# Optimization experiments

Measured on AMD Instinct MI355X. Metric: run time of the kernel, lower is better.

Reference implementation:

```python
import jax, jax.numpy as jnp
import numpy as np

B, S, C = 8, 2048, 1024
DROPOUT_RATE = 0.1


def setup_inputs() -> dict:
    key = jax.random.key(0)
    k1, k2, k3 = jax.random.split(key, 3)
    x = jax.random.normal(k1, (B, S, C), dtype=jnp.float32)
    # Fixed orthogonal projection buffer, as in __init__: U from SVD of a random matrix
    rand_mat = jax.random.normal(k2, (C, C), dtype=jnp.float32)
    U, _, _ = jnp.linalg.svd(rand_mat)
    U = U.astype(jnp.float32)
    # Base random permutation of [0, C)
    perm = jax.random.permutation(k3, C).astype(jnp.int32)
    # Stand-in for random.randint(0, 1000), fixed for determinism
    randint = 123
    return {"x": x, "U": U, "perm": perm, "randint": randint}


def reference(x, U, perm, randint):
    # channel_dim == -1, so the transpose in the original forward is a no-op.
    rand_scale = (DROPOUT_RATE / (1.0 - DROPOUT_RATE)) ** 0.5
    n = x.shape[-1]
    b = x.size // n
    # _randperm_like: per-row permutation ans[b_, i] = perm[i] * (6*randint*b_ + 1) mod n.
    # Reduce the multiplier mod n first so int32 arithmetic never overflows
    # (math is identical since (a*b) % n == (a*(b%n)) % n).
    batch_rand = (jnp.arange(b, dtype=jnp.int32) * (randint * 6) + 1) % n  # [b]
    ans = (perm[None, :] * batch_rand[:, None]) % n                        # [b, n]
    ans = ans.reshape(x.shape)                                             # same shape as x

    x_g = jnp.take_along_axis(x, ans, axis=-1)   # gather per-row permuted channels
    y = jnp.matmul(x_g, U)                        # shared (C,C) projection
    # scatter_(-1, ans, y) places y[..., j] at position ans[..., j]; since ans is a
    # permutation per row, this equals gathering y with the inverse permutation.
    inv = jnp.argsort(ans, axis=-1)
    x_next = jnp.take_along_axis(y, inv, axis=-1)
    return x_next * rand_scale + x
```

## Files before the change

kernel.cpp:

```cpp
#include <hip/hip_runtime.h>
#include <hip/hip_bf16.h>

#define WS_UT    ((size_t)0)
#define WS_XG    ((size_t)4*1024*1024)
#define WS_Y     ((size_t)36*1024*1024)

typedef __attribute__((ext_vector_type(8))) short short8;
typedef __attribute__((ext_vector_type(4))) float floatx4;

__device__ __forceinline__ void load_lds16(const void* g, void* l) {
  __builtin_amdgcn_global_load_lds(
      (const __attribute__((address_space(1))) void*)g,
      (__attribute__((address_space(3))) void*)l, 16, 0, 0);
}

__device__ __forceinline__ unsigned short f2bf(float f) {
  __hip_bfloat16 h = __float2bfloat16(f);
  return __builtin_bit_cast(unsigned short, h);
}
__device__ __forceinline__ float bf2f(unsigned short u) {
  return __uint_as_float(((unsigned)u) << 16);
}

__global__ void __launch_bounds__(256) prep_k(const float* __restrict__ U,
                                              unsigned short* __restrict__ ut) {
  __shared__ float tile[64][65];
  const int tn = (blockIdx.x & 15) * 64;
  const int tk = (blockIdx.x >> 4) * 64;
  const int r = threadIdx.x >> 6;
  const int c = threadIdx.x & 63;
  for (int s = 0; s < 16; ++s)
    tile[s * 4 + r][c] = U[(size_t)(tk + s * 4 + r) * 1024 + tn + c];
  __syncthreads();
  for (int s = 0; s < 16; ++s)
    ut[(size_t)(tn + s * 4 + r) * 1024 + tk + c] = f2bf(tile[c][s * 4 + r]);
}

__global__ void __launch_bounds__(256) gather_cast_k(const float* __restrict__ x,
                                                     const int* __restrict__ perm,
                                                     const int* __restrict__ prand,
                                                     unsigned short* __restrict__ xg) {
  __shared__ float xrow[4][1024];
  const int w = threadIdx.x >> 6, lane = threadIdx.x & 63;
  const int row = blockIdx.x * 4 + w;
  const unsigned mult = ((unsigned)prand[0] * 6u) & 1023u;
  const unsigned br = (((unsigned)row & 1023u) * mult + 1u) & 1023u;
  const float* xr = x + (size_t)row * 1024;
  unsigned short* xo = xg + (size_t)row * 1024;
  for (int t = 0; t < 4; ++t) {
    floatx4 v = *(const floatx4*)(xr + t * 256 + lane * 4);
    *(floatx4*)(&xrow[w][t * 256 + lane * 4]) = v;
  }
  __syncthreads();
  for (int t = 0; t < 4; ++t) {
    int i0 = t * 256 + lane * 4;
    int4 p = *(const int4*)(perm + i0);
    ushort4 o;
    o.x = f2bf(xrow[w][((unsigned)p.x * br) & 1023u]);
    o.y = f2bf(xrow[w][((unsigned)p.y * br) & 1023u]);
    o.z = f2bf(xrow[w][((unsigned)p.z * br) & 1023u]);
    o.w = f2bf(xrow[w][((unsigned)p.w * br) & 1023u]);
    *(ushort4*)(xo + i0) = o;
  }
}

__global__ void __launch_bounds__(256) gemm_k(const unsigned short* __restrict__ xg,
                                              const unsigned short* __restrict__ ut,
                                              unsigned short* __restrict__ y) {
  __shared__ __align__(16) char ldsA[16384];
  __shared__ __align__(16) char ldsB[16384];
  const int tid = threadIdx.x;
  const int w = tid >> 6, lane = tid & 63;
  const int l = blockIdx.x;
  const int xcd = l & 7;
  const int j = l >> 3;
  const int bn = (j & 7) * 128;
  const int bm = ((j >> 3) * 8 + xcd) * 128;
  const int wm = (w & 1) * 64, wn = (w >> 1) * 64;
  const int m = lane & 15, q = lane >> 4;
  const int srow = lane >> 3;
  const int sch = lane & 7;

  floatx4 acc[4][4];
  for (int i = 0; i < 4; ++i)
    for (int jj = 0; jj < 4; ++jj) acc[i][jj] = (floatx4)0.0f;

  for (int kt = 0; kt < 16; ++kt) {
    const int k0 = kt * 64;
    for (int t = 0; t < 4; ++t) {
      int row = w * 32 + t * 8 + srow;
      int sc = sch ^ (row & 7);
      load_lds16(xg + ((size_t)(bm + row) * 1024 + k0 + sc * 8),
                 ldsA + row * 128 + sch * 16);
      load_lds16(ut + ((size_t)(bn + row) * 1024 + k0 + sc * 8),
                 ldsB + row * 128 + sch * 16);
    }
    __syncthreads();
    for (int s = 0; s < 2; ++s) {
      short8 af[4], bfr[4];
      const int swz = ((s * 4 + q) ^ (m & 7)) * 16;
      for (int i = 0; i < 4; ++i)
        af[i] = *(const short8*)(ldsA + (wm + i * 16 + m) * 128 + swz);
      for (int jj = 0; jj < 4; ++jj)
        bfr[jj] = *(const short8*)(ldsB + (wn + jj * 16 + m) * 128 + swz);
      for (int i = 0; i < 4; ++i)
        for (int jj = 0; jj < 4; ++jj)
          acc[i][jj] = __builtin_amdgcn_mfma_f32_16x16x32_bf16(af[i], bfr[jj], acc[i][jj], 0, 0, 0);
    }
    __syncthreads();
  }
  for (int i = 0; i < 4; ++i) {
    int row = bm + wm + i * 16 + q * 4;
    for (int jj = 0; jj < 4; ++jj) {
      int col = bn + wn + jj * 16 + m;
      for (int r = 0; r < 4; ++r)
        y[(size_t)(row + r) * 1024 + col] = f2bf(acc[i][jj][r]);
    }
  }
}

__global__ void __launch_bounds__(256) scatter_out_k(const unsigned short* __restrict__ xg,
                                                     const unsigned short* __restrict__ y,
                                                     const int* __restrict__ perm,
                                                     const int* __restrict__ prand,
                                                     float* __restrict__ out) {
  __shared__ float obuf[4][1024];
  const int w = threadIdx.x >> 6, lane = threadIdx.x & 63;
  const int row = blockIdx.x * 4 + w;
  const unsigned mult = ((unsigned)prand[0] * 6u) & 1023u;
  const unsigned br = (((unsigned)row & 1023u) * mult + 1u) & 1023u;
  const unsigned short* yr = y + (size_t)row * 1024;
  const unsigned short* xr = xg + (size_t)row * 1024;
  for (int t = 0; t < 4; ++t) {
    int i0 = t * 256 + lane * 4;
    int4 p = *(const int4*)(perm + i0);
    ushort4 yv = *(const ushort4*)(yr + i0);
    ushort4 xv = *(const ushort4*)(xr + i0);
    obuf[w][((unsigned)p.x * br) & 1023u] = 0.3333333333333333f * bf2f(yv.x) + bf2f(xv.x);
    obuf[w][((unsigned)p.y * br) & 1023u] = 0.3333333333333333f * bf2f(yv.y) + bf2f(xv.y);
    obuf[w][((unsigned)p.z * br) & 1023u] = 0.3333333333333333f * bf2f(yv.z) + bf2f(xv.z);
    obuf[w][((unsigned)p.w * br) & 1023u] = 0.3333333333333333f * bf2f(yv.w) + bf2f(xv.w);
  }
  __syncthreads();
  float* orow = out + (size_t)row * 1024;
  for (int t = 0; t < 4; ++t) {
    int c0 = t * 256 + lane * 4;
    *(floatx4*)(orow + c0) = *(const floatx4*)(&obuf[w][c0]);
  }
}

extern "C" void kernel_launch(void* const* d_in, const int* in_sizes, int n_in,
                              void* d_out, int out_size, void* d_ws, size_t ws_size,
                              hipStream_t stream) {
  const float* x = (const float*)d_in[0];
  const float* U = (const float*)d_in[1];
  const int* perm = (const int*)d_in[2];
  const int* prand = (const int*)d_in[3];
  float* out = (float*)d_out;
  char* ws = (char*)d_ws;
  unsigned short* ut = (unsigned short*)(ws + WS_UT);
  unsigned short* xg = (unsigned short*)(ws + WS_XG);
  unsigned short* y = (unsigned short*)(ws + WS_Y);

  prep_k<<<256, 256, 0, stream>>>(U, ut);
  gather_cast_k<<<4096, 256, 0, stream>>>(x, perm, prand, xg);
  gemm_k<<<1024, 256, 0, stream>>>(xg, ut, y);
  scatter_out_k<<<4096, 256, 0, stream>>>(xg, y, perm, prand, out);
}
```

Before: 179.2 us.

## Fuse scatter-residual into GEMM epilogue and merge prep with gather kernel

The GEMM epilogue now writes fp32 outputs directly to their inverse-permuted positions, adding the residual from the original x, so the bf16 y intermediate and the separate scatter kernel are removed. The U transpose/cast and the row gather are combined into a single launch using block-index ranges. This cuts a full round trip of the intermediate through global memory and two launches. The cost is uncoalesced 4-byte scattered reads of x and writes of out in the epilogue.

New measurement: 235.8 us. 31.6% more time.

```diff
diff --git a/kernel.cpp b/kernel.cpp
--- a/kernel.cpp
+++ b/kernel.cpp
@@ -2,8 +2,7 @@
 #include <hip/hip_bf16.h>
 
 #define WS_UT    ((size_t)0)
-#define WS_XG    ((size_t)4*1024*1024)
-#define WS_Y     ((size_t)36*1024*1024)
+#define WS_XG    ((size_t)2*1024*1024)
 
 typedef __attribute__((ext_vector_type(8))) short short8;
 typedef __attribute__((ext_vector_type(4))) float floatx4;
@@ -18,31 +17,30 @@
   __hip_bfloat16 h = __float2bfloat16(f);
   return __builtin_bit_cast(unsigned short, h);
 }
-__device__ __forceinline__ float bf2f(unsigned short u) {
-  return __uint_as_float(((unsigned)u) << 16);
-}
 
-__global__ void __launch_bounds__(256) prep_k(const float* __restrict__ U,
-                                              unsigned short* __restrict__ ut) {
-  __shared__ float tile[64][65];
-  const int tn = (blockIdx.x & 15) * 64;
-  const int tk = (blockIdx.x >> 4) * 64;
-  const int r = threadIdx.x >> 6;
-  const int c = threadIdx.x & 63;
-  for (int s = 0; s < 16; ++s)
-    tile[s * 4 + r][c] = U[(size_t)(tk + s * 4 + r) * 1024 + tn + c];
-  __syncthreads();
-  for (int s = 0; s < 16; ++s)
-    ut[(size_t)(tn + s * 4 + r) * 1024 + tk + c] = f2bf(tile[c][s * 4 + r]);
-}
-
-__global__ void __launch_bounds__(256) gather_cast_k(const float* __restrict__ x,
+__global__ void __launch_bounds__(256) prep_gather_k(const float* __restrict__ U,
+                                                     const float* __restrict__ x,
                                                      const int* __restrict__ perm,
                                                      const int* __restrict__ prand,
+                                                     unsigned short* __restrict__ ut,
                                                      unsigned short* __restrict__ xg) {
-  __shared__ float xrow[4][1024];
+  __shared__ __align__(16) char smem[64 * 65 * 4];
+  if (blockIdx.x < 256) {
+    float (*tile)[65] = (float (*)[65])smem;
+    const int tn = (blockIdx.x & 15) * 64;
+    const int tk = (blockIdx.x >> 4) * 64;
+    const int r = threadIdx.x >> 6;
+    const int c = threadIdx.x & 63;
+    for (int s = 0; s < 16; ++s)
+      tile[s * 4 + r][c] = U[(size_t)(tk + s * 4 + r) * 1024 + tn + c];
+    __syncthreads();
+    for (int s = 0; s < 16; ++s)
+      ut[(size_t)(tn + s * 4 + r) * 1024 + tk + c] = f2bf(tile[c][s * 4 + r]);
+    return;
+  }
+  float (*xrow)[1024] = (float (*)[1024])smem;
   const int w = threadIdx.x >> 6, lane = threadIdx.x & 63;
-  const int row = blockIdx.x * 4 + w;
+  const int row = (blockIdx.x - 256) * 4 + w;
   const unsigned mult = ((unsigned)prand[0] * 6u) & 1023u;
   const unsigned br = (((unsigned)row & 1023u) * mult + 1u) & 1023u;
   const float* xr = x + (size_t)row * 1024;
@@ -64,9 +62,12 @@
   }
 }
 
-__global__ void __launch_bounds__(256) gemm_k(const unsigned short* __restrict__ xg,
-                                              const unsigned short* __restrict__ ut,
-                                              unsigned short* __restrict__ y) {
+__global__ void __launch_bounds__(256) gemm_scatter_k(const unsigned short* __restrict__ xg,
+                                                      const unsigned short* __restrict__ ut,
+                                                      const float* __restrict__ x,
+                                                      const int* __restrict__ perm,
+                                                      const int* __restrict__ prand,
+                                                      float* __restrict__ out) {
   __shared__ __align__(16) char ldsA[16384];
   __shared__ __align__(16) char ldsB[16384];
   const int tid = threadIdx.x;
@@ -109,43 +110,23 @@
     }
     __syncthreads();
   }
+
+  const unsigned mult = ((unsigned)prand[0] * 6u) & 1023u;
+  unsigned pcol[4];
+  for (int jj = 0; jj < 4; ++jj)
+    pcol[jj] = (unsigned)perm[bn + wn + jj * 16 + m];
   for (int i = 0; i < 4; ++i) {
-    int row = bm + wm + i * 16 + q * 4;
-    for (int jj = 0; jj < 4; ++jj) {
-      int col = bn + wn + jj * 16 + m;
-      for (int r = 0; r < 4; ++r)
-        y[(size_t)(row + r) * 1024 + col] = f2bf(acc[i][jj][r]);
+    const int rowb = bm + wm + i * 16 + q * 4;
+    for (int r = 0; r < 4; ++r) {
+      const int row = rowb + r;
+      const unsigned br = (((unsigned)row & 1023u) * mult + 1u) & 1023u;
+      const float* xr = x + (size_t)row * 1024;
+      float* orow = out + (size_t)row * 1024;
+      for (int jj = 0; jj < 4; ++jj) {
+        const unsigned tc = (pcol[jj] * br) & 1023u;
+        orow[tc] = 0.3333333333333333f * acc[i][jj][r] + xr[tc];
+      }
     }
-  }
-}
-
-__global__ void __launch_bounds__(256) scatter_out_k(const unsigned short* __restrict__ xg,
-                                                     const unsigned short* __restrict__ y,
-                                                     const int* __restrict__ perm,
-                                                     const int* __restrict__ prand,
-                                                     float* __restrict__ out) {
-  __shared__ float obuf[4][1024];
-  const int w = threadIdx.x >> 6, lane = threadIdx.x & 63;
-  const int row = blockIdx.x * 4 + w;
-  const unsigned mult = ((unsigned)prand[0] * 6u) & 1023u;
-  const unsigned br = (((unsigned)row & 1023u) * mult + 1u) & 1023u;
-  const unsigned short* yr = y + (size_t)row * 1024;
-  const unsigned short* xr = xg + (size_t)row * 1024;
-  for (int t = 0; t < 4; ++t) {
-    int i0 = t * 256 + lane * 4;
-    int4 p = *(const int4*)(perm + i0);
-    ushort4 yv = *(const ushort4*)(yr + i0);
-    ushort4 xv = *(const ushort4*)(xr + i0);
-    obuf[w][((unsigned)p.x * br) & 1023u] = 0.3333333333333333f * bf2f(yv.x) + bf2f(xv.x);
-    obuf[w][((unsigned)p.y * br) & 1023u] = 0.3333333333333333f * bf2f(yv.y) + bf2f(xv.y);
-    obuf[w][((unsigned)p.z * br) & 1023u] = 0.3333333333333333f * bf2f(yv.z) + bf2f(xv.z);
-    obuf[w][((unsigned)p.w * br) & 1023u] = 0.3333333333333333f * bf2f(yv.w) + bf2f(xv.w);
-  }
-  __syncthreads();
-  float* orow = out + (size_t)row * 1024;
-  for (int t = 0; t < 4; ++t) {
-    int c0 = t * 256 + lane * 4;
-    *(floatx4*)(orow + c0) = *(const floatx4*)(&obuf[w][c0]);
   }
 }
 
@@ -160,10 +141,7 @@
   char* ws = (char*)d_ws;
   unsigned short* ut = (unsigned short*)(ws + WS_UT);
   unsigned short* xg = (unsigned short*)(ws + WS_XG);
-  unsigned short* y = (unsigned short*)(ws + WS_Y);
 
-  prep_k<<<256, 256, 0, stream>>>(U, ut);
-  gather_cast_k<<<4096, 256, 0, stream>>>(x, perm, prand, xg);
-  gemm_k<<<1024, 256, 0, stream>>>(xg, ut, y);
-  scatter_out_k<<<4096, 256, 0, stream>>>(xg, y, perm, prand, out);
+  prep_gather_k<<<256 + 4096, 256, 0, stream>>>(U, x, perm, prand, ut, xg);
+  gemm_scatter_k<<<1024, 256, 0, stream>>>(xg, ut, x, perm, prand, out);
 }
```
